# Performance work log

Hardware: AMD Instinct MI355X
Metric: run time of the kernel (lower is better)

## Reference

```python
import jax, jax.numpy as jnp
import numpy as np

LAMBD = 1.0


def setup_inputs() -> dict:
    key = jax.random.key(0)
    k1, k2 = jax.random.split(key)
    B, C = 8192, 256
    x = jax.random.normal(k1, (B, C), dtype=jnp.float32)
    y = jax.random.normal(k2, (B, C), dtype=jnp.float32)
    return {"x": x, "y": y, "L": 100}


def reference(x, y, L):
    B, C = x.shape
    # Pairwise squared euclidean cost: [B, B]
    cost = (x ** 2).sum(-1, keepdims=True) - 2.0 * (x @ y.T) + (y ** 2).sum(-1)
    K = -cost * LAMBD
    log_u = jnp.zeros((B,), dtype=x.dtype)
    log_v = jnp.zeros((B,), dtype=x.dtype)

    def body(i, carry):
        log_u, log_v = carry
        # log_a = log_b = 0 (uniform-unnormalized marginals as in the original)
        log_u = -jax.scipy.special.logsumexp(K + log_v[None, :], axis=1)
        log_v = -jax.scipy.special.logsumexp(K + log_u[:, None], axis=0)
        return (log_u, log_v)

    log_u, log_v = jax.lax.fori_loop(0, L, body, (log_u, log_v))
    P = jnp.exp(log_u[:, None] + K + log_v[None, :])
    # Row-wise hard one-hot of the transport plan (argmax), then barycentric map P @ y
    one_hot = jax.nn.one_hot(jnp.argmax(P, axis=-1), B, dtype=P.dtype)
    return one_hot @ y
```

## Files before the change

### kernel.cpp

```cpp
#include <hip/hip_runtime.h>
#include <math.h>


#define B 8192
#define C 256
#define LITERS 100
#define RPB 16
#define NCH (B / RPB)

#define QS 65536.0f
#define QI 3.0517578125e-5f

typedef float f32x4 __attribute__((ext_vector_type(4)));
typedef unsigned short u16x8 __attribute__((ext_vector_type(8)));
typedef signed char i8x16 __attribute__((ext_vector_type(16)));
typedef signed char i8x8 __attribute__((ext_vector_type(8)));

__device__ __align__(16) float g_V[B];

__global__ __launch_bounds__(256) void init_V(const float* __restrict__ y) {
    int wave = threadIdx.x >> 6;
    int lane = threadIdx.x & 63;
    int row = blockIdx.x * 4 + wave;
    const f32x4* yr = (const f32x4*)(y + (size_t)row * C);
    f32x4 v = yr[lane];
    float s = v.x * v.x + v.y * v.y + v.z * v.z + v.w * v.w;
    #pragma unroll
    for (int off = 32; off; off >>= 1) s += __shfl_down(s, off, 64);
    if (lane == 0) g_V[row] = -s;
}

#define GT 64
#define GKT 64
#define LSTR (GKT + 4)

__global__ __launch_bounds__(256) void gemm_G(const float* __restrict__ x,
                                              const float* __restrict__ y,
                                              unsigned short* __restrict__ Glo,
                                              signed char* __restrict__ Ghi) {
    __shared__ float As[GT][LSTR];
    __shared__ float Bs[GT][LSTR];
    int bi = blockIdx.y * GT;
    int bj = blockIdx.x * GT;
    int t = threadIdx.x;
    int tx = t & 15, ty = t >> 4;
    float acc[4][4] = {};
    for (int kk = 0; kk < C; kk += GKT) {
        #pragma unroll
        for (int l = 0; l < 4; ++l) {
            int idx = t + l * 256;
            int r = idx >> 4;
            int c4 = idx & 15;
            *(f32x4*)&As[r][c4 * 4] =
                *(const f32x4*)(x + (size_t)(bi + r) * C + kk + c4 * 4);
            *(f32x4*)&Bs[r][c4 * 4] =
                *(const f32x4*)(y + (size_t)(bj + r) * C + kk + c4 * 4);
        }
        __syncthreads();
        #pragma unroll
        for (int k4 = 0; k4 < GKT / 4; ++k4) {
            f32x4 a[4], b[4];
            #pragma unroll
            for (int ii = 0; ii < 4; ++ii)
                a[ii] = *(const f32x4*)&As[ty * 4 + ii][k4 * 4];
            #pragma unroll
            for (int jj = 0; jj < 4; ++jj)
                b[jj] = *(const f32x4*)&Bs[tx + 16 * jj][k4 * 4];
            #pragma unroll
            for (int ii = 0; ii < 4; ++ii)
                #pragma unroll
                for (int jj = 0; jj < 4; ++jj) {
                    acc[ii][jj] = fmaf(a[ii].x, b[jj].x, acc[ii][jj]);
                    acc[ii][jj] = fmaf(a[ii].y, b[jj].y, acc[ii][jj]);
                    acc[ii][jj] = fmaf(a[ii].z, b[jj].z, acc[ii][jj]);
                    acc[ii][jj] = fmaf(a[ii].w, b[jj].w, acc[ii][jj]);
                }
        }
        __syncthreads();
    }
    #pragma unroll
    for (int ii = 0; ii < 4; ++ii) {
        int gi = bi + ty * 4 + ii;
        #pragma unroll
        for (int jj = 0; jj < 4; ++jj) {
            size_t idx = (size_t)gi * B + bj + tx + 16 * jj;
            float gs = acc[ii][jj] * QS;
            gs = fminf(fmaxf(gs, -8388607.0f), 8388607.0f);
            int v = __float2int_rn(gs);
            Glo[idx] = (unsigned short)(v & 0xFFFF);
            Ghi[idx] = (signed char)(v >> 16);
        }
    }
}

__global__ __launch_bounds__(512, 4) void fused_iter(
        const unsigned short* __restrict__ Glo,
        const signed char* __restrict__ Ghi,
        float* __restrict__ pm) {
    __shared__ float wm[2][2][8];
    __shared__ float ws[2][2][8];
    int t = threadIdx.x;
    int chunk = blockIdx.x;
    int i0 = chunk * RPB;
    int wave = t >> 6, lane = t & 63;

    float vreg[16];
    #pragma unroll
    for (int q = 0; q < 4; ++q) {
        f32x4 v = *(const f32x4*)&g_V[16 * t + 4 * q];
        vreg[4 * q + 0] = v.x; vreg[4 * q + 1] = v.y;
        vreg[4 * q + 2] = v.z; vreg[4 * q + 3] = v.w;
    }
    float cs[16];
    #pragma unroll
    for (int k = 0; k < 16; ++k) cs[k] = 0.0f;

    for (int w = 0; w < RPB / 2; ++w) {
        int buf = w & 1;
        int ra = i0 + 2 * w;
        int rb = ra + 1;
        float val0[16], val1[16];
        {
            const u16x8* lop = (const u16x8*)(Glo + (size_t)ra * B);
            const i8x16* hp  = (const i8x16*)(Ghi + (size_t)ra * B);
            u16x8 a0 = lop[2 * t], a1 = lop[2 * t + 1];
            i8x16 h = hp[t];
            #pragma unroll
            for (int e = 0; e < 8; ++e) {
                int q0 = ((int)h[e] << 16) | (int)a0[e];
                val0[e] = fmaf((float)q0, QI, vreg[e]);
                int q1 = ((int)h[8 + e] << 16) | (int)a1[e];
                val0[8 + e] = fmaf((float)q1, QI, vreg[8 + e]);
            }
        }
        {
            const u16x8* lop = (const u16x8*)(Glo + (size_t)rb * B);
            const i8x16* hp  = (const i8x16*)(Ghi + (size_t)rb * B);
            u16x8 a0 = lop[2 * t], a1 = lop[2 * t + 1];
            i8x16 h = hp[t];
            #pragma unroll
            for (int e = 0; e < 8; ++e) {
                int q0 = ((int)h[e] << 16) | (int)a0[e];
                val1[e] = fmaf((float)q0, QI, vreg[e]);
                int q1 = ((int)h[8 + e] << 16) | (int)a1[e];
                val1[8 + e] = fmaf((float)q1, QI, vreg[8 + e]);
            }
        }
        float M0 = val0[0], M1 = val1[0];
        #pragma unroll
        for (int k = 1; k < 16; ++k) {
            M0 = fmaxf(M0, val0[k]);
            M1 = fmaxf(M1, val1[k]);
        }
        #pragma unroll
        for (int off = 1; off < 64; off <<= 1) {
            M0 = fmaxf(M0, __shfl_xor(M0, off, 64));
            M1 = fmaxf(M1, __shfl_xor(M1, off, 64));
        }
        float s0 = 0.0f, s1 = 0.0f;
        #pragma unroll
        for (int k = 0; k < 16; ++k) {
            val0[k] = __expf(val0[k] - M0); s0 += val0[k];
            val1[k] = __expf(val1[k] - M1); s1 += val1[k];
        }
        #pragma unroll
        for (int off = 1; off < 64; off <<= 1) {
            s0 += __shfl_xor(s0, off, 64);
            s1 += __shfl_xor(s1, off, 64);
        }
        if (lane == 0) {
            wm[buf][0][wave] = M0; ws[buf][0][wave] = s0;
            wm[buf][1][wave] = M1; ws[buf][1][wave] = s1;
        }
        __syncthreads();
        float gM0 = wm[buf][0][0], gM1 = wm[buf][1][0];
        #pragma unroll
        for (int k = 1; k < 8; ++k) {
            gM0 = fmaxf(gM0, wm[buf][0][k]);
            gM1 = fmaxf(gM1, wm[buf][1][k]);
        }
        float gS0 = 0.0f, gS1 = 0.0f;
        #pragma unroll
        for (int k = 0; k < 8; ++k) {
            gS0 += ws[buf][0][k] * __expf(wm[buf][0][k] - gM0);
            gS1 += ws[buf][1][k] * __expf(wm[buf][1][k] - gM1);
        }
        float f0 = __expf(M0 - gM0) / gS0;
        float f1 = __expf(M1 - gM1) / gS1;
        #pragma unroll
        for (int k = 0; k < 16; ++k) {
            cs[k] = fmaf(val0[k], f0, cs[k]);
            cs[k] = fmaf(val1[k], f1, cs[k]);
        }
    }
    #pragma unroll
    for (int q = 0; q < 4; ++q) {
        f32x4 o = {cs[4 * q + 0], cs[4 * q + 1], cs[4 * q + 2], cs[4 * q + 3]};
        *(f32x4*)&pm[(size_t)chunk * B + 16 * t + 4 * q] = o;
    }
}

__global__ __launch_bounds__(256) void col_combine(const float* __restrict__ pm) {
    int t = threadIdx.x;
    int pl = t & 31;
    int g = t >> 5;
    int j = blockIdx.x * 32 + pl;
    float s = 0.0f;
    #pragma unroll 8
    for (int c = g * 64; c < g * 64 + 64; ++c)
        s += pm[(size_t)c * B + j];
    __shared__ float ls[8][32];
    ls[g][pl] = s;
    __syncthreads();
    if (t < 32) {
        float s0 = ls[0][t];
        #pragma unroll
        for (int gg = 1; gg < 8; ++gg) s0 += ls[gg][t];
        int jj = blockIdx.x * 32 + t;
        g_V[jj] -= logf(fmaxf(s0, 1e-30f));
    }
}

__global__ __launch_bounds__(256) void argmax_out(const unsigned short* __restrict__ Glo,
                                                  const signed char* __restrict__ Ghi,
                                                  const float* __restrict__ y,
                                                  float* __restrict__ out) {
    int i = blockIdx.x;
    int t = threadIdx.x;
    const u16x8* lo8 = (const u16x8*)(Glo + (size_t)i * B);
    const i8x8*  hi8 = (const i8x8*)(Ghi + (size_t)i * B);
    const f32x4* v4 = (const f32x4*)g_V;
    float best = -INFINITY;
    int bj = 0;
    #pragma unroll
    for (int it = 0; it < 4; ++it) {
        int idx = it * 256 + t;
        u16x8 lo = lo8[idx];
        i8x8  hi = hi8[idx];
        f32x4 va = v4[idx * 2], vb = v4[idx * 2 + 1];
        float vv[8] = {va.x, va.y, va.z, va.w, vb.x, vb.y, vb.z, vb.w};
        #pragma unroll
        for (int k = 0; k < 8; ++k) {
            int q = ((int)hi[k] << 16) | (int)lo[k];
            float val = fmaf((float)q, QI, vv[k]);
            int j = idx * 8 + k;
            if (val > best) { best = val; bj = j; }
        }
    }
    __shared__ float bm[256];
    __shared__ int   bidx[256];
    bm[t] = best; bidx[t] = bj;
    __syncthreads();
    #pragma unroll
    for (int off = 128; off; off >>= 1) {
        if (t < off) {
            float om = bm[t + off]; int oj = bidx[t + off];
            if (om > bm[t] || (om == bm[t] && oj < bidx[t])) { bm[t] = om; bidx[t] = oj; }
        }
        __syncthreads();
    }
    int jstar = bidx[0];
    out[(size_t)i * C + t] = y[(size_t)jstar * C + t];
}

extern "C" void kernel_launch(void* const* d_in, const int* in_sizes, int n_in,
                              void* d_out, int out_size, void* d_ws, size_t ws_size,
                              hipStream_t stream) {
    const float* x = (const float*)d_in[0];
    const float* y = (const float*)d_in[1];
    float* out = (float*)d_out;
    unsigned short* Glo = (unsigned short*)d_ws;
    signed char*    Ghi = (signed char*)((char*)d_ws + (size_t)B * B * 2);
    float* pm = (float*)((char*)d_ws + (size_t)B * B * 3);

    init_V<<<B / 4, 256, 0, stream>>>(y);
    gemm_G<<<dim3(B / GT, B / GT), 256, 0, stream>>>(x, y, Glo, Ghi);
    for (int l = 0; l < LITERS; ++l) {
        fused_iter<<<NCH, 512, 0, stream>>>(Glo, Ghi, pm);
        col_combine<<<B / 32, 256, 0, stream>>>(pm);
    }
    argmax_out<<<B, 256, 0, stream>>>(Glo, Ghi, y, out);
}
```

Baseline: 4.875 ms.

## Replace most dense Sinkhorn iterations with thresholded sparse row iterations

After a handful of dense iterations, each row's entries within a tau margin of its log-sum-exp are extracted into a per-row sparse list capped at KMAX. Most of the 100 Sinkhorn iterations then run over these sparse lists with LDS atomics for the column sums, and the lists are re-extracted after a dense refresh in each of four phases. This cuts the bandwidth and exp work of scanning the full quantized 8192x8192 matrix every iteration. It approximates the logsumexp by dropping entries below the threshold, and the dense/sparse iteration schedule is hand-tuned, so the result may drift from the exact reference.

```diff
diff --git a/kernel.cpp b/kernel.cpp
--- a/kernel.cpp
+++ b/kernel.cpp
@@ -4,9 +4,11 @@
 
 #define B 8192
 #define C 256
-#define LITERS 100
 #define RPB 16
-#define NCH (B / RPB)
+#define NCH 512
+#define KMAX 1024
+#define SROWS 32
+#define SNCH (B / SROWS)
 
 #define QS 65536.0f
 #define QI 3.0517578125e-5f
@@ -17,6 +19,7 @@
 typedef signed char i8x8 __attribute__((ext_vector_type(8)));
 
 __device__ __align__(16) float g_V[B];
+__device__ int g_cnt[B];
 
 __global__ __launch_bounds__(256) void init_V(const float* __restrict__ y) {
     int wave = threadIdx.x >> 6;
@@ -200,14 +203,15 @@
     }
 }
 
-__global__ __launch_bounds__(256) void col_combine(const float* __restrict__ pm) {
+__global__ __launch_bounds__(256) void col_combine(const float* __restrict__ pm,
+                                                   int nch, int freeze0) {
     int t = threadIdx.x;
     int pl = t & 31;
     int g = t >> 5;
     int j = blockIdx.x * 32 + pl;
+    int per = nch >> 3;
     float s = 0.0f;
-    #pragma unroll 8
-    for (int c = g * 64; c < g * 64 + 64; ++c)
+    for (int c = g * per; c < (g + 1) * per; ++c)
         s += pm[(size_t)c * B + j];
     __shared__ float ls[8][32];
     ls[g][pl] = s;
@@ -217,7 +221,142 @@
         #pragma unroll
         for (int gg = 1; gg < 8; ++gg) s0 += ls[gg][t];
         int jj = blockIdx.x * 32 + t;
-        g_V[jj] -= logf(fmaxf(s0, 1e-30f));
+        if (!(freeze0 && s0 == 0.0f))
+            g_V[jj] -= logf(fmaxf(s0, 1e-30f));
+    }
+}
+
+__global__ __launch_bounds__(512, 2) void extract_sparse(
+        const unsigned short* __restrict__ Glo,
+        const signed char* __restrict__ Ghi,
+        unsigned short* __restrict__ sidx,
+        unsigned short* __restrict__ svlo,
+        signed char* __restrict__ svhi) {
+    __shared__ float V_lds[B];
+    int t = threadIdx.x;
+    int wave = t >> 6, lane = t & 63;
+    #pragma unroll
+    for (int k = 0; k < 4; ++k) {
+        int fi = 2048 * k + 4 * t;
+        *(f32x4*)&V_lds[fi] = *(const f32x4*)&g_V[fi];
+    }
+    __syncthreads();
+
+    int row = blockIdx.x * 8 + wave;
+    const u16x8* lop = (const u16x8*)(Glo + (size_t)row * B);
+    const i8x8*  hp  = (const i8x8*)(Ghi + (size_t)row * B);
+
+    float m = -1e30f, s = 0.0f;
+    for (int c = 0; c < 16; ++c) {
+        int vi = c * 64 + lane;
+        u16x8 lo = lop[vi];
+        i8x8  hi = hp[vi];
+        #pragma unroll
+        for (int e = 0; e < 8; ++e) {
+            int q = ((int)hi[e] << 16) | (int)lo[e];
+            float val = fmaf((float)q, QI, V_lds[vi * 8 + e]);
+            float d = val - m;
+            float E = __expf(-fabsf(d));
+            bool nm = d > 0.0f;
+            s = nm ? fmaf(s, E, 1.0f) : (s + E);
+            m = nm ? val : m;
+        }
+    }
+    #pragma unroll
+    for (int off = 1; off < 64; off <<= 1) {
+        float mo = __shfl_xor(m, off, 64), so = __shfl_xor(s, off, 64);
+        float m2 = fmaxf(m, mo);
+        s = s * __expf(m - m2) + so * __expf(mo - m2);
+        m = m2;
+    }
+    float W = m + logf(s);
+
+    unsigned long long lanelt = (1ULL << lane) - 1ULL;
+    float tau = 80.0f;
+    int cnt = 0;
+    for (int attempt = 0; attempt < 5; ++attempt) {
+        cnt = 0;
+        float thresh = W - tau;
+        for (int c = 0; c < 16; ++c) {
+            int vi = c * 64 + lane;
+            u16x8 lo = lop[vi];
+            i8x8  hi = hp[vi];
+            #pragma unroll
+            for (int e = 0; e < 8; ++e) {
+                int q = ((int)hi[e] << 16) | (int)lo[e];
+                float val = fmaf((float)q, QI, V_lds[vi * 8 + e]);
+                bool keep = val > thresh;
+                unsigned long long mask = __ballot(keep);
+                int pos = cnt + __popcll(mask & lanelt);
+                if (keep && pos < KMAX) {
+                    size_t o = (size_t)row * KMAX + pos;
+                    sidx[o] = (unsigned short)(vi * 8 + e);
+                    svlo[o] = (unsigned short)(q & 0xFFFF);
+                    svhi[o] = (signed char)(q >> 16);
+                }
+                cnt += (int)__popcll(mask);
+            }
+        }
+        if (cnt <= KMAX) break;
+        tau -= 16.0f;
+    }
+    if (lane == 0) g_cnt[row] = (cnt < KMAX) ? cnt : KMAX;
+}
+
+__global__ __launch_bounds__(512, 2) void sparse_iter(
+        const unsigned short* __restrict__ sidx,
+        const unsigned short* __restrict__ svlo,
+        const signed char* __restrict__ svhi,
+        float* __restrict__ pm) {
+    __shared__ float V_lds[B];
+    __shared__ float csum[B];
+    int t = threadIdx.x;
+    int wave = t >> 6, lane = t & 63;
+    #pragma unroll
+    for (int k = 0; k < 4; ++k) {
+        int fi = 2048 * k + 4 * t;
+        *(f32x4*)&V_lds[fi] = *(const f32x4*)&g_V[fi];
+        *(f32x4*)&csum[fi] = f32x4{0.f, 0.f, 0.f, 0.f};
+    }
+    __syncthreads();
+
+    int base = blockIdx.x * SROWS;
+    for (int q = 0; q < 4; ++q) {
+        int row = base + wave * 4 + q;
+        int cnt = g_cnt[row];
+        const unsigned short* sip = sidx + (size_t)row * KMAX;
+        const unsigned short* slp = svlo + (size_t)row * KMAX;
+        const signed char*    shp = svhi + (size_t)row * KMAX;
+        float m = -1e30f, s = 0.0f;
+        for (int e = lane; e < cnt; e += 64) {
+            int qv = ((int)shp[e] << 16) | (int)slp[e];
+            float val = fmaf((float)qv, QI, V_lds[sip[e]]);
+            float d = val - m;
+            float E = __expf(-fabsf(d));
+            bool nm = d > 0.0f;
+            s = nm ? fmaf(s, E, 1.0f) : (s + E);
+            m = nm ? val : m;
+        }
+        #pragma unroll
+        for (int off = 1; off < 64; off <<= 1) {
+            float mo = __shfl_xor(m, off, 64), so = __shfl_xor(s, off, 64);
+            float m2 = fmaxf(m, mo);
+            s = s * __expf(m - m2) + so * __expf(mo - m2);
+            m = m2;
+        }
+        float W = m + logf(s);
+        for (int e = lane; e < cnt; e += 64) {
+            int j = sip[e];
+            int qv = ((int)shp[e] << 16) | (int)slp[e];
+            float val = fmaf((float)qv, QI, V_lds[j]);
+            atomicAdd(&csum[j], __expf(val - W));
+        }
+    }
+    __syncthreads();
+    #pragma unroll
+    for (int k = 0; k < 4; ++k) {
+        int fi = 2048 * k + 4 * t;
+        *(f32x4*)&pm[(size_t)blockIdx.x * B + fi] = *(const f32x4*)&csum[fi];
     }
 }
 
@@ -269,15 +408,29 @@
     const float* x = (const float*)d_in[0];
     const float* y = (const float*)d_in[1];
     float* out = (float*)d_out;
-    unsigned short* Glo = (unsigned short*)d_ws;
-    signed char*    Ghi = (signed char*)((char*)d_ws + (size_t)B * B * 2);
-    float* pm = (float*)((char*)d_ws + (size_t)B * B * 3);
+    char* w = (char*)d_ws;
+    unsigned short* Glo = (unsigned short*)w;
+    signed char*    Ghi = (signed char*)(w + (size_t)B * B * 2);
+    float* pm = (float*)(w + (size_t)B * B * 3);
+    unsigned short* sidx = (unsigned short*)(w + (size_t)B * B * 3 + (size_t)NCH * B * 4);
+    unsigned short* svlo = (unsigned short*)((char*)sidx + (size_t)B * KMAX * 2);
+    signed char*    svhi = (signed char*)((char*)svlo + (size_t)B * KMAX * 2);
 
     init_V<<<B / 4, 256, 0, stream>>>(y);
     gemm_G<<<dim3(B / GT, B / GT), 256, 0, stream>>>(x, y, Glo, Ghi);
-    for (int l = 0; l < LITERS; ++l) {
-        fused_iter<<<NCH, 512, 0, stream>>>(Glo, Ghi, pm);
-        col_combine<<<B / 32, 256, 0, stream>>>(pm);
+
+    const int dense_runs[4]  = {8, 1, 1, 1};
+    const int sparse_runs[4] = {24, 23, 23, 19};
+    for (int ph = 0; ph < 4; ++ph) {
+        for (int l = 0; l < dense_runs[ph]; ++l) {
+            fused_iter<<<NCH, 512, 0, stream>>>(Glo, Ghi, pm);
+            col_combine<<<B / 32, 256, 0, stream>>>(pm, NCH, 0);
+        }
+        extract_sparse<<<B / 8, 512, 0, stream>>>(Glo, Ghi, sidx, svlo, svhi);
+        for (int l = 0; l < sparse_runs[ph]; ++l) {
+            sparse_iter<<<SNCH, 512, 0, stream>>>(sidx, svlo, svhi, pm);
+            col_combine<<<B / 32, 256, 0, stream>>>(pm, SNCH, 1);
+        }
     }
     argmax_out<<<B, 256, 0, stream>>>(Glo, Ghi, y, out);
 }
```

New measurement: 7.033 ms. +44.3%, slower.

## Switch most Sinkhorn iterations to thresholded sparse CSR/CSC log-sum-exp updates

Applied to the files above, without the earlier changes.

After a few dense Sinkhorn iterations, each row's significant entries (within a log-margin of the row log-sum-exp) are extracted into a compact row-major list. They are then transposed into a column-major layout via atomic counting and a prefix scan. Subsequent row and column updates run over only these sparse entries, and the sparsity pattern is re-extracted periodically. This avoids streaming the full quantized cost matrix every iteration, at the risk of truncation error if significant entries are dropped or capped at KMAX.

```diff
diff --git a/kernel.cpp b/kernel.cpp
--- a/kernel.cpp
+++ b/kernel.cpp
@@ -4,9 +4,11 @@
 
 #define B 8192
 #define C 256
-#define LITERS 100
 #define RPB 16
 #define NCH (B / RPB)
+#define KMAX 768
+#define NMAX (B * KMAX)
+#define TAU 80.0f
 
 #define QS 65536.0f
 #define QI 3.0517578125e-5f
@@ -17,6 +19,8 @@
 typedef signed char i8x8 __attribute__((ext_vector_type(8)));
 
 __device__ __align__(16) float g_V[B];
+__device__ __align__(16) float g_W[B];
+__device__ int g_rowcnt[B], g_colcnt[B], g_colofs[B];
 
 __global__ __launch_bounds__(256) void init_V(const float* __restrict__ y) {
     int wave = threadIdx.x >> 6;
@@ -221,6 +225,201 @@
     }
 }
 
+__global__ __launch_bounds__(256) void sreset() {
+    int i = blockIdx.x * 256 + threadIdx.x;
+    g_colcnt[i] = 0;
+}
+
+__global__ __launch_bounds__(512, 2) void extract(
+        const unsigned short* __restrict__ Glo,
+        const signed char* __restrict__ Ghi,
+        unsigned short* __restrict__ cidx,
+        unsigned short* __restrict__ clo,
+        signed char* __restrict__ chi) {
+    int t = threadIdx.x;
+    int wave = t >> 6, lane = t & 63;
+    int row = blockIdx.x * 8 + wave;
+    const u16x8* lop = (const u16x8*)(Glo + (size_t)row * B);
+    const i8x8*  hp  = (const i8x8*)(Ghi + (size_t)row * B);
+
+    float m = -1e30f, s = 0.0f;
+    for (int c = 0; c < 16; ++c) {
+        int vi = c * 64 + lane;
+        u16x8 lo = lop[vi];
+        i8x8  hi = hp[vi];
+        #pragma unroll
+        for (int e = 0; e < 8; ++e) {
+            int q = ((int)hi[e] << 16) | (int)lo[e];
+            float val = fmaf((float)q, QI, g_V[vi * 8 + e]);
+            float d = val - m;
+            float E = __expf(-fabsf(d));
+            bool nm = d > 0.0f;
+            s = nm ? fmaf(s, E, 1.0f) : (s + E);
+            m = nm ? val : m;
+        }
+    }
+    #pragma unroll
+    for (int off = 1; off < 64; off <<= 1) {
+        float mo = __shfl_xor(m, off, 64), so = __shfl_xor(s, off, 64);
+        float m2 = fmaxf(m, mo);
+        s = s * __expf(m - m2) + so * __expf(mo - m2);
+        m = m2;
+    }
+    float W = m + logf(s);
+
+    float tau = TAU;
+    int cnt = 0;
+    for (int att = 0; att < 5; ++att) {
+        cnt = 0;
+        float th = W - tau;
+        for (int c = 0; c < 16; ++c) {
+            int vi = c * 64 + lane;
+            u16x8 lo = lop[vi];
+            i8x8  hi = hp[vi];
+            #pragma unroll
+            for (int e = 0; e < 8; ++e) {
+                int q = ((int)hi[e] << 16) | (int)lo[e];
+                float val = fmaf((float)q, QI, g_V[vi * 8 + e]);
+                cnt += (int)__popcll(__ballot(val > th));
+            }
+        }
+        if (cnt <= KMAX) break;
+        tau -= 16.0f;
+    }
+    float th = W - tau;
+
+    unsigned long long lanelt = (1ULL << lane) - 1ULL;
+    int base = row * KMAX;
+    int off0 = 0;
+    for (int c = 0; c < 16; ++c) {
+        int vi = c * 64 + lane;
+        u16x8 lo = lop[vi];
+        i8x8  hi = hp[vi];
+        #pragma unroll
+        for (int e = 0; e < 8; ++e) {
+            int q = ((int)hi[e] << 16) | (int)lo[e];
+            float val = fmaf((float)q, QI, g_V[vi * 8 + e]);
+            bool keep = val > th;
+            unsigned long long mask = __ballot(keep);
+            int pos = off0 + (int)__popcll(mask & lanelt);
+            if (keep && pos < KMAX) {
+                int j = vi * 8 + e;
+                cidx[base + pos] = (unsigned short)j;
+                clo[base + pos] = lo[e];
+                chi[base + pos] = hi[e];
+                atomicAdd(&g_colcnt[j], 1);
+            }
+            off0 += (int)__popcll(mask);
+        }
+    }
+    if (lane == 0) g_rowcnt[row] = (cnt < KMAX) ? cnt : KMAX;
+}
+
+__global__ __launch_bounds__(1024) void col_prefix() {
+    __shared__ int ls[1024];
+    int t = threadIdx.x;
+    int c[8], sum = 0;
+    #pragma unroll
+    for (int k = 0; k < 8; ++k) { c[k] = g_colcnt[t * 8 + k]; sum += c[k]; }
+    ls[t] = sum;
+    __syncthreads();
+    for (int off = 1; off < 1024; off <<= 1) {
+        int add = (t >= off) ? ls[t - off] : 0;
+        __syncthreads();
+        ls[t] += add;
+        __syncthreads();
+    }
+    int run = (t == 0) ? 0 : ls[t - 1];
+    #pragma unroll
+    for (int k = 0; k < 8; ++k) {
+        g_colofs[t * 8 + k] = run;
+        run += c[k];
+        g_colcnt[t * 8 + k] = 0;
+    }
+}
+
+__global__ __launch_bounds__(512, 2) void build_csc(
+        const unsigned short* __restrict__ cidx,
+        const unsigned short* __restrict__ clo,
+        const signed char* __restrict__ chi,
+        unsigned short* __restrict__ ridx,
+        unsigned short* __restrict__ rlo,
+        signed char* __restrict__ rhi) {
+    int t = threadIdx.x;
+    int wave = t >> 6, lane = t & 63;
+    int row = blockIdx.x * 8 + wave;
+    int cnt = g_rowcnt[row];
+    cnt = (cnt < KMAX) ? cnt : KMAX;
+    int base = row * KMAX;
+    for (int e = lane; e < cnt; e += 64) {
+        int p = base + e;
+        int j = (int)cidx[p] & (B - 1);
+        int slot = atomicAdd(&g_colcnt[j], 1);
+        int o = g_colofs[j] + slot;
+        o = (o < NMAX) ? o : (NMAX - 1);
+        o = (o >= 0) ? o : 0;
+        ridx[o] = (unsigned short)row;
+        rlo[o] = clo[p];
+        rhi[o] = chi[p];
+    }
+}
+
+__global__ __launch_bounds__(512) void sparse_W(
+        const unsigned short* __restrict__ cidx,
+        const unsigned short* __restrict__ clo,
+        const signed char* __restrict__ chi) {
+    int t = threadIdx.x;
+    int wave = t >> 6, lane = t & 63;
+    int row = blockIdx.x * 8 + wave;
+    int cnt = g_rowcnt[row];
+    cnt = (cnt < KMAX) ? cnt : KMAX;
+    int base = row * KMAX;
+    float m = -1e30f;
+    for (int e = lane; e < cnt; e += 64) {
+        int p = base + e;
+        int q = ((int)chi[p] << 16) | (int)clo[p];
+        m = fmaxf(m, fmaf((float)q, QI, g_V[(int)cidx[p] & (B - 1)]));
+    }
+    #pragma unroll
+    for (int off = 1; off < 64; off <<= 1)
+        m = fmaxf(m, __shfl_xor(m, off, 64));
+    float s = 0.0f;
+    for (int e = lane; e < cnt; e += 64) {
+        int p = base + e;
+        int q = ((int)chi[p] << 16) | (int)clo[p];
+        s += __expf(fmaf((float)q, QI, g_V[(int)cidx[p] & (B - 1)]) - m);
+    }
+    #pragma unroll
+    for (int off = 1; off < 64; off <<= 1)
+        s += __shfl_xor(s, off, 64);
+    if (lane == 0) g_W[row] = m + logf(s);
+}
+
+__global__ __launch_bounds__(512) void sparse_colV(
+        const unsigned short* __restrict__ ridx,
+        const unsigned short* __restrict__ rlo,
+        const signed char* __restrict__ rhi) {
+    int t = threadIdx.x;
+    int wave = t >> 6, lane = t & 63;
+    int col = blockIdx.x * 8 + wave;
+    int cnt = g_colcnt[col];
+    int base = g_colofs[col];
+    if (base < 0) base = 0;
+    if (base + cnt > NMAX) cnt = NMAX - base;
+    float vj = g_V[col];
+    float s = 0.0f;
+    for (int e = lane; e < cnt; e += 64) {
+        int p = base + e;
+        int q = ((int)rhi[p] << 16) | (int)rlo[p];
+        s += __expf(fmaf((float)q, QI, vj) - g_W[(int)ridx[p] & (B - 1)]);
+    }
+    #pragma unroll
+    for (int off = 1; off < 64; off <<= 1)
+        s += __shfl_xor(s, off, 64);
+    if (lane == 0 && cnt > 0)
+        g_V[col] = vj - logf(fmaxf(s, 1e-30f));
+}
+
 __global__ __launch_bounds__(256) void argmax_out(const unsigned short* __restrict__ Glo,
                                                   const signed char* __restrict__ Ghi,
                                                   const float* __restrict__ y,
@@ -259,7 +458,7 @@
         }
         __syncthreads();
     }
-    int jstar = bidx[0];
+    int jstar = bidx[0] & (B - 1);
     out[(size_t)i * C + t] = y[(size_t)jstar * C + t];
 }
 
@@ -269,15 +468,33 @@
     const float* x = (const float*)d_in[0];
     const float* y = (const float*)d_in[1];
     float* out = (float*)d_out;
-    unsigned short* Glo = (unsigned short*)d_ws;
-    signed char*    Ghi = (signed char*)((char*)d_ws + (size_t)B * B * 2);
-    float* pm = (float*)((char*)d_ws + (size_t)B * B * 3);
+    char* w = (char*)d_ws;
+    unsigned short* Glo = (unsigned short*)w;
+    signed char*    Ghi = (signed char*)(w + (size_t)B * B * 2);
+    float* pm = (float*)(w + (size_t)B * B * 3);
+    unsigned short* cidx = (unsigned short*)(w + (size_t)B * B * 3);
+    unsigned short* clo  = (unsigned short*)((char*)cidx + (size_t)NMAX * 2);
+    signed char*    chi  = (signed char*)((char*)clo + (size_t)NMAX * 2);
+    unsigned short* ridx = (unsigned short*)((char*)chi + (size_t)NMAX);
+    unsigned short* rlo  = (unsigned short*)((char*)ridx + (size_t)NMAX * 2);
+    signed char*    rhi  = (signed char*)((char*)rlo + (size_t)NMAX * 2);
 
     init_V<<<B / 4, 256, 0, stream>>>(y);
     gemm_G<<<dim3(B / GT, B / GT), 256, 0, stream>>>(x, y, Glo, Ghi);
-    for (int l = 0; l < LITERS; ++l) {
+
+    for (int l = 0; l < 8; ++l) {
         fused_iter<<<NCH, 512, 0, stream>>>(Glo, Ghi, pm);
         col_combine<<<B / 32, 256, 0, stream>>>(pm);
     }
+    for (int ph = 0; ph < 4; ++ph) {
+        sreset<<<B / 256, 256, 0, stream>>>();
+        extract<<<B / 8, 512, 0, stream>>>(Glo, Ghi, cidx, clo, chi);
+        col_prefix<<<1, 1024, 0, stream>>>();
+        build_csc<<<B / 8, 512, 0, stream>>>(cidx, clo, chi, ridx, rlo, rhi);
+        for (int l = 0; l < 23; ++l) {
+            sparse_W<<<B / 8, 512, 0, stream>>>(cidx, clo, chi);
+            sparse_colV<<<B / 8, 512, 0, stream>>>(ridx, rlo, rhi);
+        }
+    }
     argmax_out<<<B, 256, 0, stream>>>(Glo, Ghi, y, out);
 }
```

After: 7.049 ms. 1.45x slower.
